# Performance work log

Hardware: AMD Instinct MI355X
Metric: run time of the kernel (lower is better)

The kernel has to match this reference:

```python
import jax, jax.numpy as jnp
import numpy as np
import math


def _bandwidth(d):
    # gz = 2*Gamma((d+1)/2)/Gamma(d/2); use lgamma for numerical stability.
    gz = 2.0 * math.exp(math.lgamma(0.5 * (d + 1)) - math.lgamma(0.5 * d))
    return 1.0 / (2.0 * gz * gz)


def _kernel_mean(xa, xb, gamma):
    # mean over the [Na, Nb] RBF kernel matrix, squared distance via matmul identity
    sq = (jnp.sum(xa * xa, axis=1)[:, None]
          + jnp.sum(xb * xb, axis=1)[None, :]
          - 2.0 * (xa @ xb.T))
    sq = jnp.maximum(sq, 0.0)  # guard tiny negatives from the identity
    return jnp.mean(jnp.exp(-gamma * sq))


def setup_inputs() -> dict:
    key = jax.random.key(0)
    k1, k2 = jax.random.split(key)
    x1 = jax.random.normal(k1, (8192, 128), dtype=jnp.float32)
    x2 = jax.random.normal(k2, (8192, 128), dtype=jnp.float32)
    return {"x1": x1, "x2": x2}


def reference(x1, x2):
    g1 = _bandwidth(x1.shape[1])
    g2 = _bandwidth(x2.shape[1])
    m11 = _kernel_mean(x1, x1, g1)
    m22 = _kernel_mean(x2, x2, g2)
    m12 = _kernel_mean(x1, x2, g1)
    return jnp.sqrt(m11 - 2.0 * m12 + m22)
```

## Files before the change

kernel.cpp:

```cpp
#include <hip/hip_runtime.h>
#include <cmath>

#define D 128
#define BM 128
#define BN 64
#define NSEG 12
#define LOG2E 1.4426950408889634

typedef __attribute__((ext_vector_type(8))) _Float16 f16x8;
typedef __attribute__((ext_vector_type(4))) float f32x4;
typedef __attribute__((ext_vector_type(2))) float f32x2;

__device__ __forceinline__ void async_cp16(const void* g, void* l) {
    __builtin_amdgcn_global_load_lds(
        (__attribute__((address_space(1))) void*)g,
        (__attribute__((address_space(3))) void*)l, 16, 0, 0);
}

__global__ __launch_bounds__(256) void prep_kernel(
    const float* __restrict__ x1, const float* __restrict__ x2,
    _Float16* __restrict__ xh, float* __restrict__ El,
    double* __restrict__ acc, float gl, int N) {
    int tid = threadIdx.x;
    if (blockIdx.x == 0 && tid < 64) acc[tid] = 0.0;
    int r = blockIdx.x * 16 + (tid >> 4);
    if (r >= 2 * N) return;
    int l = tid & 15;
    const float* row = (r < N) ? x1 + (size_t)r * D : x2 + (size_t)(r - N) * D;
    float4 v0 = ((const float4*)row)[l * 2];
    float4 v1 = ((const float4*)row)[l * 2 + 1];
    float v[8] = {v0.x, v0.y, v0.z, v0.w, v1.x, v1.y, v1.z, v1.w};
    float p = 0.f;
    _Float16 h8[8];
#pragma unroll
    for (int j = 0; j < 8; ++j) {
        p = fmaf(v[j], v[j], p);
        h8[j] = (_Float16)v[j];
    }
    *(uint4*)(xh + (size_t)r * D + l * 8) = *(uint4*)h8;
#pragma unroll
    for (int off = 8; off; off >>= 1) p += __shfl_down(p, off, 16);
    if (l == 0) El[r] = gl * p;
}

__global__ __launch_bounds__(256, 3) void mmd_mfma_kernel(
    const _Float16* __restrict__ xh, const float* __restrict__ El,
    double* __restrict__ acc, float c2l, int N) {
    __shared__ float4 smem[2][1024];

    int tid = threadIdx.x;
    int lane = tid & 63, wave = tid >> 6;
    int quad = lane >> 4, l16 = lane & 15;
    int wrow = (wave & 1) * 64;
    int wcol = (wave >> 1) * 32;

    int nt2 = 2 * N / BM;
    int half = N / BM;
    int p = blockIdx.x / NSEG;
    int s = blockIdx.x % NSEG;
    int tpp = nt2 + 1;
    int q = tpp / NSEG, r = tpp % NSEG;
    int t0 = s * q + (s < r ? s : r);
    int nt = q + (s < r ? 1 : 0);
    int H = 2 * nt;

    int goff[4];
#pragma unroll
    for (int i = 0; i < 4; ++i) {
        int slot = i * 256 + tid;
        int row = slot >> 4;
        int g = (slot & 15) ^ (row & 7);
        goff[i] = row * D + g * 8;
    }

    auto stage = [&](int b2Base, int buf) {
        const _Float16* src = xh + (size_t)b2Base * D;
#pragma unroll
        for (int i = 0; i < 4; ++i)
            async_cp16(src + goff[i], &smem[buf][i * 256 + tid]);
    };
    auto BI = [&](int tt) { return tt <= p ? p : nt2 - 1 - p; };
    auto BJ = [&](int tt) { return tt <= p ? tt : tt - p - 1; };

    stage(BJ(t0) * BM, 0);
    stage(BJ(t0) * BM + BN, 1);

    f16x8 a[4][4];
    float4 ea4[4];
    int curA = -1;
    double dsum = 0.0;

    for (int ht = 0; ht < H; ++ht) {
        int tt = t0 + (ht >> 1), h = ht & 1;
        int bi = BI(tt), bj = BJ(tt);
        int aBase = bi * BM;
        int bcolBase = bj * BM + h * BN;
        float w = (bi == bj) ? 1.0f : 2.0f;
        if ((bi < half) != (bj < half)) w = -2.0f;
        int cur = ht & 1;

        if (ht + 1 < H) {
            asm volatile("s_waitcnt vmcnt(4)" ::: "memory");
        } else {
            asm volatile("s_waitcnt vmcnt(0)" ::: "memory");
        }
        __builtin_amdgcn_s_barrier();
        __builtin_amdgcn_sched_barrier(0);

        int bcol0 = bcolBase + wcol + l16;
        float ebv0 = El[bcol0];
        float ebv1 = El[bcol0 + 16];

        if (aBase != curA) {
            curA = aBase;
#pragma unroll
            for (int u = 0; u < 4; ++u) {
                int ar = aBase + wrow + u * 16 + l16;
#pragma unroll
                for (int j = 0; j < 4; ++j) {
                    int g = (j >> 1) * 8 + (j & 1) * 4 + quad;
                    a[u][j] = *(const f16x8*)(xh + (size_t)ar * D + g * 8);
                }
            }
            int arow0 = aBase + wrow + quad * 4;
#pragma unroll
            for (int ti = 0; ti < 4; ++ti)
                ea4[ti] = *(const float4*)&El[arow0 + ti * 16];
        }
        __builtin_amdgcn_sched_barrier(0);

        f32x4 C[4][2];
#pragma unroll
        for (int ti = 0; ti < 4; ++ti)
#pragma unroll
            for (int tj = 0; tj < 2; ++tj) C[ti][tj] = {0.f, 0.f, 0.f, 0.f};

        __builtin_amdgcn_s_setprio(1);
#pragma unroll
        for (int j = 0; j < 4; ++j) {
            int gb = (j >> 1) * 8 + (j & 1) * 4 + quad;
            f16x8 b[2];
#pragma unroll
            for (int u = 0; u < 2; ++u) {
                int br = wcol + u * 16 + l16;
                b[u] = *(const f16x8*)&smem[cur][br * 16 + (gb ^ (br & 7))];
            }
#pragma unroll
            for (int ti = 0; ti < 4; ++ti)
#pragma unroll
                for (int tj = 0; tj < 2; ++tj)
                    C[ti][tj] = __builtin_amdgcn_mfma_f32_16x16x32_f16(
                        a[ti][j], b[tj], C[ti][tj], 0, 0, 0);
        }
        __builtin_amdgcn_s_setprio(0);

        f32x2 cc = {c2l, c2l};
        float lsum = 0.f;
#pragma unroll
        for (int tj = 0; tj < 2; ++tj) {
            f32x2 p2 = {0.f, 0.f};
#pragma unroll
            for (int ti = 0; ti < 4; ++ti) {
                f32x4 d = C[ti][tj];
                f32x2 a01 = cc * f32x2{d.x, d.y} + f32x2{ea4[ti].x, ea4[ti].y};
                f32x2 a23 = cc * f32x2{d.z, d.w} + f32x2{ea4[ti].z, ea4[ti].w};
                f32x2 e, e2;
                e.x = __builtin_amdgcn_exp2f(a01.x);
                e.y = __builtin_amdgcn_exp2f(a01.y);
                e2.x = __builtin_amdgcn_exp2f(a23.x);
                e2.y = __builtin_amdgcn_exp2f(a23.y);
                p2 += e + e2;
            }
            lsum = fmaf(p2.x + p2.y,
                        __builtin_amdgcn_exp2f(tj ? ebv1 : ebv0), lsum);
        }
        dsum += (double)lsum * (double)w;

        __builtin_amdgcn_sched_barrier(0);
        __builtin_amdgcn_s_barrier();
        __builtin_amdgcn_sched_barrier(0);
        if (ht + 2 < H) {
            int tn = t0 + ((ht + 2) >> 1);
            stage(BJ(tn) * BM + h * BN, cur);
        }
    }

#pragma unroll
    for (int off = 32; off; off >>= 1) dsum += __shfl_down(dsum, off);
    double* red = (double*)&smem[0][0];
    if (lane == 0) red[wave] = dsum;
    __syncthreads();
    if (tid == 0)
        atomicAdd(&acc[blockIdx.x & 63], red[0] + red[1] + red[2] + red[3]);
}

__global__ __launch_bounds__(64) void mmd_finalize_kernel(
    const double* __restrict__ acc, float* __restrict__ out, int N) {
    int l = threadIdx.x;
    double v = acc[l];
#pragma unroll
    for (int off = 32; off; off >>= 1) v += __shfl_down(v, off);
    if (l == 0) {
        double nn = (double)N * (double)N;
        double s = v / nn;
        out[0] = (float)sqrt(s > 0.0 ? s : 0.0);
    }
}

extern "C" void kernel_launch(void* const* d_in, const int* in_sizes, int n_in,
                              void* d_out, int out_size, void* d_ws, size_t ws_size,
                              hipStream_t stream) {
    const float* x1 = (const float*)d_in[0];
    const float* x2 = (const float*)d_in[1];
    int N = in_sizes[0] / D;

    double* acc = (double*)d_ws;
    float* El = (float*)((char*)d_ws + 8192);
    _Float16* xh = (_Float16*)((char*)d_ws + 73728);

    double lg = lgamma(0.5 * (D + 1)) - lgamma(0.5 * D);
    double gz = 2.0 * exp(lg);
    double gamma = 1.0 / (2.0 * gz * gz);
    float gl = (float)(-gamma * LOG2E);
    float c2l = (float)(2.0 * gamma * LOG2E);

    prep_kernel<<<(2 * N + 15) / 16, 256, 0, stream>>>(x1, x2, xh, El, acc, gl, N);

    int nblocks = 64 * NSEG;
    mmd_mfma_kernel<<<nblocks, 256, 0, stream>>>(xh, El, acc, c2l, N);

    mmd_finalize_kernel<<<1, 64, 0, stream>>>(acc, (float*)d_out, N);
}
```

Measured before the change: 105.9 us.

## Load B tiles directly from global memory instead of LDS double-buffering

Removes the async global-to-LDS double-buffered staging of the B tile, along with its barriers, waitcnt and setprio. Each wave now reads its B fragments straight from global memory, relying on L1/L2 caching. This drops LDS traffic and block-wide synchronisation. In exchange, B data shared by two waves is fetched twice and global-load latency is exposed directly before the MFMAs with no prefetch.

```diff
diff --git a/kernel.cpp b/kernel.cpp
--- a/kernel.cpp
+++ b/kernel.cpp
@@ -10,12 +10,6 @@
 typedef __attribute__((ext_vector_type(8))) _Float16 f16x8;
 typedef __attribute__((ext_vector_type(4))) float f32x4;
 typedef __attribute__((ext_vector_type(2))) float f32x2;
-
-__device__ __forceinline__ void async_cp16(const void* g, void* l) {
-    __builtin_amdgcn_global_load_lds(
-        (__attribute__((address_space(1))) void*)g,
-        (__attribute__((address_space(3))) void*)l, 16, 0, 0);
-}
 
 __global__ __launch_bounds__(256) void prep_kernel(
     const float* __restrict__ x1, const float* __restrict__ x2,
@@ -46,7 +40,7 @@
 __global__ __launch_bounds__(256, 3) void mmd_mfma_kernel(
     const _Float16* __restrict__ xh, const float* __restrict__ El,
     double* __restrict__ acc, float c2l, int N) {
-    __shared__ float4 smem[2][1024];
+    __shared__ double red[4];
 
     int tid = threadIdx.x;
     int lane = tid & 63, wave = tid >> 6;
@@ -64,26 +58,8 @@
     int nt = q + (s < r ? 1 : 0);
     int H = 2 * nt;
 
-    int goff[4];
-#pragma unroll
-    for (int i = 0; i < 4; ++i) {
-        int slot = i * 256 + tid;
-        int row = slot >> 4;
-        int g = (slot & 15) ^ (row & 7);
-        goff[i] = row * D + g * 8;
-    }
-
-    auto stage = [&](int b2Base, int buf) {
-        const _Float16* src = xh + (size_t)b2Base * D;
-#pragma unroll
-        for (int i = 0; i < 4; ++i)
-            async_cp16(src + goff[i], &smem[buf][i * 256 + tid]);
-    };
     auto BI = [&](int tt) { return tt <= p ? p : nt2 - 1 - p; };
     auto BJ = [&](int tt) { return tt <= p ? tt : tt - p - 1; };
-
-    stage(BJ(t0) * BM, 0);
-    stage(BJ(t0) * BM + BN, 1);
 
     f16x8 a[4][4];
     float4 ea4[4];
@@ -97,19 +73,6 @@
         int bcolBase = bj * BM + h * BN;
         float w = (bi == bj) ? 1.0f : 2.0f;
         if ((bi < half) != (bj < half)) w = -2.0f;
-        int cur = ht & 1;
-
-        if (ht + 1 < H) {
-            asm volatile("s_waitcnt vmcnt(4)" ::: "memory");
-        } else {
-            asm volatile("s_waitcnt vmcnt(0)" ::: "memory");
-        }
-        __builtin_amdgcn_s_barrier();
-        __builtin_amdgcn_sched_barrier(0);
-
-        int bcol0 = bcolBase + wcol + l16;
-        float ebv0 = El[bcol0];
-        float ebv1 = El[bcol0 + 16];
 
         if (aBase != curA) {
             curA = aBase;
@@ -127,7 +90,10 @@
             for (int ti = 0; ti < 4; ++ti)
                 ea4[ti] = *(const float4*)&El[arow0 + ti * 16];
         }
-        __builtin_amdgcn_sched_barrier(0);
+
+        int bcol0 = bcolBase + wcol + l16;
+        float ebv0 = El[bcol0];
+        float ebv1 = El[bcol0 + 16];
 
         f32x4 C[4][2];
 #pragma unroll
@@ -135,15 +101,14 @@
 #pragma unroll
             for (int tj = 0; tj < 2; ++tj) C[ti][tj] = {0.f, 0.f, 0.f, 0.f};
 
-        __builtin_amdgcn_s_setprio(1);
 #pragma unroll
         for (int j = 0; j < 4; ++j) {
             int gb = (j >> 1) * 8 + (j & 1) * 4 + quad;
             f16x8 b[2];
 #pragma unroll
             for (int u = 0; u < 2; ++u) {
-                int br = wcol + u * 16 + l16;
-                b[u] = *(const f16x8*)&smem[cur][br * 16 + (gb ^ (br & 7))];
+                int br = bcolBase + wcol + u * 16 + l16;
+                b[u] = *(const f16x8*)(xh + (size_t)br * D + gb * 8);
             }
 #pragma unroll
             for (int ti = 0; ti < 4; ++ti)
@@ -152,7 +117,6 @@
                     C[ti][tj] = __builtin_amdgcn_mfma_f32_16x16x32_f16(
                         a[ti][j], b[tj], C[ti][tj], 0, 0, 0);
         }
-        __builtin_amdgcn_s_setprio(0);
 
         f32x2 cc = {c2l, c2l};
         float lsum = 0.f;
@@ -175,19 +139,10 @@
                         __builtin_amdgcn_exp2f(tj ? ebv1 : ebv0), lsum);
         }
         dsum += (double)lsum * (double)w;
-
-        __builtin_amdgcn_sched_barrier(0);
-        __builtin_amdgcn_s_barrier();
-        __builtin_amdgcn_sched_barrier(0);
-        if (ht + 2 < H) {
-            int tn = t0 + ((ht + 2) >> 1);
-            stage(BJ(tn) * BM + h * BN, cur);
-        }
     }
 
 #pragma unroll
     for (int off = 32; off; off >>= 1) dsum += __shfl_down(dsum, off);
-    double* red = (double*)&smem[0][0];
     if (lane == 0) red[wave] = dsum;
     __syncthreads();
     if (tid == 0)
```

After: 131.0 us. +23.7%, slower.

## Software-pipeline MFMA with previous half-tile's exp epilogue using double accumulators

Applied to the files above, without the earlier changes.

Interleaves the exp2 epilogue of the previous half-tile with the MFMA chain of the current one, using two ping-pong accumulator sets so matrix and transcendental work can overlap. The loop is split into two phases by A-row block, so the A fragments are loaded once per phase and the per-iteration branch goes away. El values for A rows are now reloaded per chunk instead of held in registers. The second accumulator set raises register pressure, which could hurt occupancy at three blocks per CU, and the setprio hints are dropped.

```diff
diff --git a/kernel.cpp b/kernel.cpp
--- a/kernel.cpp
+++ b/kernel.cpp
@@ -86,14 +86,57 @@
     stage(BJ(t0) * BM + BN, 1);
 
     f16x8 a[4][4];
-    float4 ea4[4];
-    int curA = -1;
+    f32x4 CA[4][2], CB[4][2];
+    const f32x4 CZ = {0.f, 0.f, 0.f, 0.f};
+#pragma unroll
+    for (int ti = 0; ti < 4; ++ti) {
+        CA[ti][0] = CZ; CA[ti][1] = CZ;
+        CB[ti][0] = CZ; CB[ti][1] = CZ;
+    }
+
+    float ebP0 = 0.f, ebP1 = 0.f, wP = 0.f;
+    int curABase = 0;
     double dsum = 0.0;
-
-    for (int ht = 0; ht < H; ++ht) {
+    f32x2 cc = {c2l, c2l};
+
+    auto loadA = [&](int aBase) {
+        curABase = aBase;
+#pragma unroll
+        for (int u = 0; u < 4; ++u) {
+            int ar = aBase + wrow + u * 16 + l16;
+#pragma unroll
+            for (int j = 0; j < 4; ++j) {
+                int g = (j >> 1) * 8 + (j & 1) * 4 + quad;
+                a[u][j] = *(const f16x8*)(xh + (size_t)ar * D + g * 8);
+            }
+        }
+    };
+
+    auto epiChunk = [&](const f32x4& d0, const f32x4& d1, int j,
+                        f32x2& p20, f32x2& p21) {
+        float4 ea = *(const float4*)&El[curABase + wrow + j * 16 + quad * 4];
+        f32x2 eaxy = {ea.x, ea.y}, eazw = {ea.z, ea.w};
+        f32x2 a01 = cc * f32x2{d0.x, d0.y} + eaxy;
+        f32x2 a23 = cc * f32x2{d0.z, d0.w} + eazw;
+        f32x2 b01 = cc * f32x2{d1.x, d1.y} + eaxy;
+        f32x2 b23 = cc * f32x2{d1.z, d1.w} + eazw;
+        f32x2 e0, e1, e2, e3;
+        e0.x = __builtin_amdgcn_exp2f(a01.x); e0.y = __builtin_amdgcn_exp2f(a01.y);
+        e1.x = __builtin_amdgcn_exp2f(a23.x); e1.y = __builtin_amdgcn_exp2f(a23.y);
+        e2.x = __builtin_amdgcn_exp2f(b01.x); e2.y = __builtin_amdgcn_exp2f(b01.y);
+        e3.x = __builtin_amdgcn_exp2f(b23.x); e3.y = __builtin_amdgcn_exp2f(b23.y);
+        p20 += e0 + e1;
+        p21 += e2 + e3;
+    };
+    auto epiFinish = [&](f32x2 p20, f32x2 p21) {
+        float s0 = (p20.x + p20.y) * __builtin_amdgcn_exp2f(ebP0);
+        float s1 = (p21.x + p21.y) * __builtin_amdgcn_exp2f(ebP1);
+        dsum += (double)(s0 + s1) * (double)wP;
+    };
+
+    auto halfTile = [&](int ht, f32x4 (&Cc)[4][2], f32x4 (&Cp)[4][2]) {
         int tt = t0 + (ht >> 1), h = ht & 1;
         int bi = BI(tt), bj = BJ(tt);
-        int aBase = bi * BM;
         int bcolBase = bj * BM + h * BN;
         float w = (bi == bj) ? 1.0f : 2.0f;
         if ((bi < half) != (bj < half)) w = -2.0f;
@@ -108,73 +151,37 @@
         __builtin_amdgcn_sched_barrier(0);
 
         int bcol0 = bcolBase + wcol + l16;
-        float ebv0 = El[bcol0];
-        float ebv1 = El[bcol0 + 16];
-
-        if (aBase != curA) {
-            curA = aBase;
-#pragma unroll
-            for (int u = 0; u < 4; ++u) {
-                int ar = aBase + wrow + u * 16 + l16;
-#pragma unroll
-                for (int j = 0; j < 4; ++j) {
-                    int g = (j >> 1) * 8 + (j & 1) * 4 + quad;
-                    a[u][j] = *(const f16x8*)(xh + (size_t)ar * D + g * 8);
+        float ebC0 = El[bcol0];
+        float ebC1 = El[bcol0 + 16];
+
+        f32x2 p20 = {0.f, 0.f}, p21 = {0.f, 0.f};
+
+#pragma unroll
+        for (int j = 0; j < 4; ++j) {
+            int gb = (j >> 1) * 8 + (j & 1) * 4 + quad;
+            int br0 = wcol + l16, br1 = wcol + 16 + l16;
+            f16x8 b0 = *(const f16x8*)&smem[cur][br0 * 16 + (gb ^ (br0 & 7))];
+            f16x8 b1 = *(const f16x8*)&smem[cur][br1 * 16 + (gb ^ (br1 & 7))];
+            if (j == 0) {
+#pragma unroll
+                for (int ti = 0; ti < 4; ++ti) {
+                    Cc[ti][0] = __builtin_amdgcn_mfma_f32_16x16x32_f16(
+                        a[ti][0], b0, CZ, 0, 0, 0);
+                    Cc[ti][1] = __builtin_amdgcn_mfma_f32_16x16x32_f16(
+                        a[ti][0], b1, CZ, 0, 0, 0);
+                }
+            } else {
+#pragma unroll
+                for (int ti = 0; ti < 4; ++ti) {
+                    Cc[ti][0] = __builtin_amdgcn_mfma_f32_16x16x32_f16(
+                        a[ti][j], b0, Cc[ti][0], 0, 0, 0);
+                    Cc[ti][1] = __builtin_amdgcn_mfma_f32_16x16x32_f16(
+                        a[ti][j], b1, Cc[ti][1], 0, 0, 0);
                 }
             }
-            int arow0 = aBase + wrow + quad * 4;
-#pragma unroll
-            for (int ti = 0; ti < 4; ++ti)
-                ea4[ti] = *(const float4*)&El[arow0 + ti * 16];
-        }
-        __builtin_amdgcn_sched_barrier(0);
-
-        f32x4 C[4][2];
-#pragma unroll
-        for (int ti = 0; ti < 4; ++ti)
-#pragma unroll
-            for (int tj = 0; tj < 2; ++tj) C[ti][tj] = {0.f, 0.f, 0.f, 0.f};
-
-        __builtin_amdgcn_s_setprio(1);
-#pragma unroll
-        for (int j = 0; j < 4; ++j) {
-            int gb = (j >> 1) * 8 + (j & 1) * 4 + quad;
-            f16x8 b[2];
-#pragma unroll
-            for (int u = 0; u < 2; ++u) {
-                int br = wcol + u * 16 + l16;
-                b[u] = *(const f16x8*)&smem[cur][br * 16 + (gb ^ (br & 7))];
-            }
-#pragma unroll
-            for (int ti = 0; ti < 4; ++ti)
-#pragma unroll
-                for (int tj = 0; tj < 2; ++tj)
-                    C[ti][tj] = __builtin_amdgcn_mfma_f32_16x16x32_f16(
-                        a[ti][j], b[tj], C[ti][tj], 0, 0, 0);
-        }
-        __builtin_amdgcn_s_setprio(0);
-
-        f32x2 cc = {c2l, c2l};
-        float lsum = 0.f;
-#pragma unroll
-        for (int tj = 0; tj < 2; ++tj) {
-            f32x2 p2 = {0.f, 0.f};
-#pragma unroll
-            for (int ti = 0; ti < 4; ++ti) {
-                f32x4 d = C[ti][tj];
-                f32x2 a01 = cc * f32x2{d.x, d.y} + f32x2{ea4[ti].x, ea4[ti].y};
-                f32x2 a23 = cc * f32x2{d.z, d.w} + f32x2{ea4[ti].z, ea4[ti].w};
-                f32x2 e, e2;
-                e.x = __builtin_amdgcn_exp2f(a01.x);
-                e.y = __builtin_amdgcn_exp2f(a01.y);
-                e2.x = __builtin_amdgcn_exp2f(a23.x);
-                e2.y = __builtin_amdgcn_exp2f(a23.y);
-                p2 += e + e2;
-            }
-            lsum = fmaf(p2.x + p2.y,
-                        __builtin_amdgcn_exp2f(tj ? ebv1 : ebv0), lsum);
-        }
-        dsum += (double)lsum * (double)w;
+            epiChunk(Cp[j][0], Cp[j][1], j, p20, p21);
+        }
+        epiFinish(p20, p21);
 
         __builtin_amdgcn_sched_barrier(0);
         __builtin_amdgcn_s_barrier();
@@ -183,6 +190,37 @@
             int tn = t0 + ((ht + 2) >> 1);
             stage(BJ(tn) * BM + h * BN, cur);
         }
+        wP = w; ebP0 = ebC0; ebP1 = ebC1;
+    };
+
+    auto drain = [&](f32x4 (&Cp)[4][2]) {
+        f32x2 p20 = {0.f, 0.f}, p21 = {0.f, 0.f};
+#pragma unroll
+        for (int j = 0; j < 4; ++j) epiChunk(Cp[j][0], Cp[j][1], j, p20, p21);
+        epiFinish(p20, p21);
+    };
+
+    int tiles1 = p + 1 - t0;
+    if (tiles1 < 0) tiles1 = 0;
+    if (tiles1 > nt) tiles1 = nt;
+    int H1 = 2 * tiles1;
+
+    if (H1 > 0) {
+        loadA(p * BM);
+        for (int k = 0; k < H1; k += 2) {
+            halfTile(k, CA, CB);
+            halfTile(k + 1, CB, CA);
+        }
+        drain(CB);
+        wP = 0.f;
+    }
+    if (H1 < H) {
+        loadA((nt2 - 1 - p) * BM);
+        for (int k = H1; k < H; k += 2) {
+            halfTile(k, CA, CB);
+            halfTile(k + 1, CB, CA);
+        }
+        drain(CB);
     }
 
 #pragma unroll
```

Measured after the change: 225.9 us. 2.13x slower.
